# Kernel tuning notes

Measured on AMD Instinct MI355X. Metric: run time of the kernel, lower is better.

The kernel has to match this reference:

```python
import jax, jax.numpy as jnp
import numpy as np

B, S, DIM = 8, 1, 2048
H = 16
QLR, KVLR = 1536, 512
DN, DR, DV = 128, 64, 128      # qk_nope, qk_rope, v head dims
START = 8191                    # start_pos; end_pos = START + S = 8192
EPS = 1e-6
SCALE = (DN + DR) ** -0.5


def _rms(x, w):
    # F.rms_norm: x / sqrt(mean(x^2)+eps) * w
    return x * w * jax.lax.rsqrt(jnp.mean(jnp.square(x), axis=-1, keepdims=True) + EPS)


def _rope(x, cos, sin):
    # x: [..., r]; consecutive pairs (x0,x1) treated as complex, multiplied by cos+i*sin
    xr, xi = x[..., 0::2], x[..., 1::2]
    out_r = xr * cos - xi * sin
    out_i = xr * sin + xi * cos
    return jnp.stack([out_r, out_i], axis=-1).reshape(x.shape)


def setup_inputs() -> dict:
    key = jax.random.key(0)
    ks = jax.random.split(key, 12)
    # rotary tables for the single decode position
    inv_freq = 1.0 / (10000.0 ** (np.arange(0, DR, 2, dtype=np.float32) / DR))  # [DR/2]
    pos = np.arange(START, START + S, dtype=np.float32)[:, None]                # [S,1]
    ang = pos * inv_freq[None, :]                                               # [S, DR/2]
    return {
        "x": jax.random.normal(ks[0], (B, S, DIM), jnp.float32),
        "start_pos": START,
        "freqs_cos": jnp.asarray(np.cos(ang)),
        "freqs_sin": jnp.asarray(np.sin(ang)),
        "kv_cache_prefix": jax.random.normal(ks[1], (B, START, KVLR), jnp.float32),
        "pe_cache_prefix": jax.random.normal(ks[2], (B, START, DR), jnp.float32),
        "wq_a_w": jax.random.normal(ks[3], (QLR, DIM), jnp.float32) * 0.02,
        "wq_a_b": jnp.zeros((QLR,), jnp.float32),
        "q_norm_w": jnp.ones((QLR,), jnp.float32),
        "wq_b_w": jax.random.normal(ks[4], (H * (DN + DR), QLR), jnp.float32) * 0.02,
        "wq_b_b": jnp.zeros((H * (DN + DR),), jnp.float32),
        "wkv_a_w": jax.random.normal(ks[5], (KVLR + DR, DIM), jnp.float32) * 0.02,
        "wkv_a_b": jnp.zeros((KVLR + DR,), jnp.float32),
        "kv_norm_w": jnp.ones((KVLR,), jnp.float32),
        "wkv_b_w": jax.random.normal(ks[6], (H * (DN + DV), KVLR), jnp.float32) * 0.02,
        "wo_w": jax.random.normal(ks[7], (DIM, H * DV), jnp.float32) * 0.02,
        "wo_b": jnp.zeros((DIM,), jnp.float32),
    }


def reference(x, start_pos, freqs_cos, freqs_sin, kv_cache_prefix, pe_cache_prefix,
              wq_a_w, wq_a_b, q_norm_w, wq_b_w, wq_b_b,
              wkv_a_w, wkv_a_b, kv_norm_w, wkv_b_w, wo_w, wo_b):
    b, s, _ = x.shape
    # low-rank query projection
    q = _rms(x @ wq_a_w.T + wq_a_b, q_norm_w) @ wq_b_w.T + wq_b_b
    q = q.reshape(b, s, H, DN + DR)
    q_nope, q_pe = q[..., :DN], q[..., DN:]
    cos = freqs_cos[None, :, None, :]  # [1,s,1,DR/2]
    sin = freqs_sin[None, :, None, :]
    q_pe = _rope(q_pe, cos, sin)
    # compressed KV + rope key branch
    kvpe = x @ wkv_a_w.T + wkv_a_b               # [b,s,KVLR+DR]
    kv, k_pe = kvpe[..., :KVLR], kvpe[..., KVLR:]
    k_pe = _rope(k_pe[:, :, None, :], cos, sin)[:, :, 0, :]
    # weight absorption: project q_nope into latent space through wkv_b's K-part
    wkv_b = wkv_b_w.reshape(H, DN + DV, KVLR)
    q_abs = jnp.einsum('bshd,hdc->bshc', q_nope, wkv_b[:, :DN])
    # append current step to caches
    kv_cache = jnp.concatenate([kv_cache_prefix, _rms(kv, kv_norm_w)], axis=1)  # [b,t,KVLR]
    pe_cache = jnp.concatenate([pe_cache_prefix, k_pe], axis=1)                 # [b,t,DR]
    # attention in latent space (seqlen=1 decode -> no causal mask needed)
    scores = (jnp.einsum('bshc,btc->bsht', q_abs, kv_cache)
              + jnp.einsum('bshr,btr->bsht', q_pe, pe_cache)) * SCALE
    attn = jax.nn.softmax(scores.astype(jnp.float32), axis=-1).astype(x.dtype)
    out = jnp.einsum('bsht,btc->bshc', attn, kv_cache)
    out = jnp.einsum('bshc,hdc->bshd', out, wkv_b[:, DN:])  # V-part of wkv_b
    return out.reshape(b, s, H * DV) @ wo_w.T + wo_b
```

## Files before the change

### kernel.cpp

```cpp
#include <hip/hip_runtime.h>
#include <math.h>

namespace {
constexpr int B_   = 8;
constexpr int DIM_ = 2048;
constexpr int H_   = 16;
constexpr int QLR_ = 1536;
constexpr int KVLR_= 512;
constexpr int DN_  = 128;
constexpr int DR_  = 64;
constexpr int DV_  = 128;
constexpr int TPRE_= 8191;
constexpr int CE_  = 576;
constexpr int NCH_ = 32;
constexpr int CT_  = 256;
constexpr int TS_  = 32;
constexpr int PSTR_= 20;
constexpr float EPS_ = 1e-6f;
constexpr float SCALE_ = 0.07216878364870322f;

constexpr size_t WS_QLAT  = 0;
constexpr size_t WS_KVPE  = WS_QLAT  + (size_t)B_*QLR_;
constexpr size_t WS_KVNEW = WS_KVPE  + (size_t)B_*CE_;
constexpr size_t WS_PENEW = WS_KVNEW + (size_t)B_*KVLR_;
constexpr size_t WS_QRS   = WS_PENEW + (size_t)B_*DR_;
constexpr size_t WS_QNOPE = WS_QRS   + (size_t)B_;
constexpr size_t WS_QT    = WS_QNOPE + (size_t)B_*H_*DN_;
constexpr size_t WS_MLOC  = WS_QT    + (size_t)B_*CE_*H_;
constexpr size_t WS_LLOC  = WS_MLOC  + (size_t)B_*H_*NCH_;
constexpr size_t WS_OUT2  = WS_LLOC  + (size_t)B_*H_*NCH_;
constexpr size_t WS_OPART = WS_OUT2  + (size_t)B_*DIM_;
}

__device__ __forceinline__ void gload16(const float* src, float* ldsDst) {
  __builtin_amdgcn_global_load_lds((const __attribute__((address_space(1))) void*)src,
                                   (__attribute__((address_space(3))) void*)ldsDst,
                                   16, 0, 0);
}

__device__ __forceinline__ float rsum16(float v) {
  int x = __float_as_int(v);
  v += __int_as_float(__builtin_amdgcn_update_dpp(0, x, 0xB1, 0xF, 0xF, true));
  x = __float_as_int(v);
  v += __int_as_float(__builtin_amdgcn_update_dpp(0, x, 0x4E, 0xF, 0xF, true));
  x = __float_as_int(v);
  v += __int_as_float(__builtin_amdgcn_update_dpp(0, x, 0x141, 0xF, 0xF, true));
  x = __float_as_int(v);
  v += __int_as_float(__builtin_amdgcn_update_dpp(0, x, 0x140, 0xF, 0xF, true));
  return v;
}

__global__ __launch_bounds__(256) void mla_k1(const float* __restrict__ x,
                                              const float* __restrict__ wqa,
                                              const float* __restrict__ bqa,
                                              const float* __restrict__ wkva,
                                              const float* __restrict__ bkva,
                                              float* __restrict__ ws) {
  const int w = threadIdx.x >> 6, l = threadIdx.x & 63;
  const int r = blockIdx.x * 4 + w;
  const float* W; const float* bias; float* out; int rr; int ostride;
  if (r < QLR_) { W = wqa;  bias = bqa;  out = ws + WS_QLAT; rr = r;        ostride = QLR_; }
  else          { W = wkva; bias = bkva; out = ws + WS_KVPE; rr = r - QLR_; ostride = CE_;  }
  const float4* wp = (const float4*)(W + (size_t)rr * DIM_);
  const float4* x4 = (const float4*)x;
  float4 wv[8];
#pragma unroll
  for (int j = 0; j < 8; ++j) wv[j] = wp[l + 64 * j];
  float acc[B_];
#pragma unroll
  for (int b = 0; b < B_; ++b) acc[b] = 0.f;
#pragma unroll
  for (int b = 0; b < B_; ++b) {
#pragma unroll
    for (int j = 0; j < 8; ++j) {
      const float4 xv = x4[b * (DIM_ / 4) + l + 64 * j];
      acc[b] = fmaf(wv[j].x, xv.x, fmaf(wv[j].y, xv.y, fmaf(wv[j].z, xv.z, fmaf(wv[j].w, xv.w, acc[b]))));
    }
  }
#pragma unroll
  for (int b = 0; b < B_; ++b)
#pragma unroll
    for (int s = 32; s; s >>= 1) acc[b] += __shfl_xor(acc[b], s);
  if (l == 0) {
    const float b0 = bias[rr];
#pragma unroll
    for (int b = 0; b < B_; ++b) out[b * ostride + rr] = acc[b] + b0;
  }
}

__global__ __launch_bounds__(256) void mla_k2(const float* __restrict__ kvnw,
                                              const float* __restrict__ fcos,
                                              const float* __restrict__ fsin,
                                              float* __restrict__ ws) {
  const int tid = threadIdx.x;
  const int b = tid >> 5, i = tid & 31;
  const float* kvpe = ws + WS_KVPE + b * CE_;
  float ss = 0.f;
#pragma unroll
  for (int j = 0; j < KVLR_ / 32; ++j) { const float v = kvpe[i + 32 * j]; ss = fmaf(v, v, ss); }
#pragma unroll
  for (int s = 16; s; s >>= 1) ss += __shfl_xor(ss, s, 32);
  const float scale = 1.0f / sqrtf(ss / (float)KVLR_ + EPS_);
  float* kvn = ws + WS_KVNEW + b * KVLR_;
#pragma unroll
  for (int j = 0; j < KVLR_ / 32; ++j) {
    const int c = i + 32 * j;
    kvn[c] = kvpe[c] * kvnw[c] * scale;
  }
  {
    const float xr = kvpe[KVLR_ + 2 * i], xi = kvpe[KVLR_ + 2 * i + 1];
    const float c = fcos[i], s = fsin[i];
    float* pen = ws + WS_PENEW + b * DR_;
    pen[2 * i]     = xr * c - xi * s;
    pen[2 * i + 1] = xr * s + xi * c;
  }
  {
    const float* p = ws + WS_QLAT + b * QLR_;
    float sq = 0.f;
#pragma unroll
    for (int j = 0; j < QLR_ / 32; ++j) { const float v = p[i + 32 * j]; sq = fmaf(v, v, sq); }
#pragma unroll
    for (int s = 16; s; s >>= 1) sq += __shfl_xor(sq, s, 32);
    if (i == 0) ws[WS_QRS + b] = 1.0f / sqrtf(sq / (float)QLR_ + EPS_);
  }
}

__global__ __launch_bounds__(256) void mla_k3(const float* __restrict__ qnw,
                                              const float* __restrict__ wqb,
                                              const float* __restrict__ bqb,
                                              const float* __restrict__ fcos,
                                              const float* __restrict__ fsin,
                                              float* __restrict__ ws) {
  const int w = threadIdx.x >> 6, l = threadIdx.x & 63;
  const int r0 = blockIdx.x * 8 + w * 2;
  const float4* w0p = (const float4*)(wqb + (size_t)r0 * QLR_);
  const float4* w1p = (const float4*)(wqb + (size_t)(r0 + 1) * QLR_);
  const float4* g4  = (const float4*)qnw;
  const float4* x4  = (const float4*)(ws + WS_QLAT);
  float4 wg0[6], wg1[6];
#pragma unroll
  for (int j = 0; j < 6; ++j) {
    const int c4 = l + 64 * j;
    const float4 a = w0p[c4], bb = w1p[c4], g = g4[c4];
    wg0[j].x = a.x * g.x; wg0[j].y = a.y * g.y; wg0[j].z = a.z * g.z; wg0[j].w = a.w * g.w;
    wg1[j].x = bb.x * g.x; wg1[j].y = bb.y * g.y; wg1[j].z = bb.z * g.z; wg1[j].w = bb.w * g.w;
  }
  float acc0[B_], acc1[B_];
#pragma unroll
  for (int b = 0; b < B_; ++b) { acc0[b] = 0.f; acc1[b] = 0.f; }
#pragma unroll
  for (int b = 0; b < B_; ++b) {
#pragma unroll
    for (int j = 0; j < 6; ++j) {
      const float4 xv = x4[b * (QLR_ / 4) + l + 64 * j];
      acc0[b] = fmaf(wg0[j].x, xv.x, fmaf(wg0[j].y, xv.y, fmaf(wg0[j].z, xv.z, fmaf(wg0[j].w, xv.w, acc0[b]))));
      acc1[b] = fmaf(wg1[j].x, xv.x, fmaf(wg1[j].y, xv.y, fmaf(wg1[j].z, xv.z, fmaf(wg1[j].w, xv.w, acc1[b]))));
    }
  }
#pragma unroll
  for (int b = 0; b < B_; ++b)
#pragma unroll
    for (int s = 32; s; s >>= 1) {
      acc0[b] += __shfl_xor(acc0[b], s);
      acc1[b] += __shfl_xor(acc1[b], s);
    }
  if (l == 0) {
    const int h = r0 / (DN_ + DR_);
    const int j0 = r0 - h * (DN_ + DR_);
    const float b0 = bqb[r0], b1 = bqb[r0 + 1];
    if (j0 < DN_) {
      float* qn = ws + WS_QNOPE;
#pragma unroll
      for (int b = 0; b < B_; ++b) {
        const float sb = ws[WS_QRS + b];
        qn[(b * H_ + h) * DN_ + j0]     = acc0[b] * sb + b0;
        qn[(b * H_ + h) * DN_ + j0 + 1] = acc1[b] * sb + b1;
      }
    } else {
      const int i = (j0 - DN_) >> 1;
      const float c = fcos[i], s = fsin[i];
      float* qTT = ws + WS_QT;
#pragma unroll
      for (int b = 0; b < B_; ++b) {
        const float sb = ws[WS_QRS + b];
        const float xr = acc0[b] * sb + b0, xi = acc1[b] * sb + b1;
        qTT[((size_t)(b * H_ + h)) * CE_ + KVLR_ + 2 * i]     = xr * c - xi * s;
        qTT[((size_t)(b * H_ + h)) * CE_ + KVLR_ + 2 * i + 1] = xr * s + xi * c;
      }
    }
  }
}

__global__ __launch_bounds__(256) void mla_k4(const float* __restrict__ wkvb,
                                              float* __restrict__ ws) {
  __shared__ float red[7 * 32 * B_];
  const int h = blockIdx.y;
  const int strip = blockIdx.x;
  const int tid = threadIdx.x;
  const int c = tid & 31, dg = tid >> 5;
  const int cg = strip * 32 + c;
  const float* qn = ws + WS_QNOPE;
  float acc[B_];
#pragma unroll
  for (int b = 0; b < B_; ++b) acc[b] = 0.f;
  const float* wp = wkvb + (size_t)h * 256 * KVLR_ + cg;
#pragma unroll
  for (int dd = 0; dd < 16; ++dd) {
    const int d = dg * 16 + dd;
    const float wv = wp[(size_t)d * KVLR_];
#pragma unroll
    for (int b = 0; b < B_; ++b) acc[b] = fmaf(qn[(b * H_ + h) * DN_ + d], wv, acc[b]);
  }
  if (dg > 0) {
#pragma unroll
    for (int b = 0; b < B_; ++b) red[(((dg - 1) * 32) + c) * B_ + b] = acc[b];
  }
  __syncthreads();
  if (dg == 0) {
    float* qTT = ws + WS_QT;
#pragma unroll
    for (int b = 0; b < B_; ++b) {
      float v = acc[b];
#pragma unroll
      for (int g = 0; g < 7; ++g) v += red[(g * 32 + c) * B_ + b];
      qTT[((size_t)(b * H_ + h)) * CE_ + cg] = v;
    }
  }
}

__global__ __launch_bounds__(512) void mla_k5(const float* __restrict__ kvpre,
                                              const float* __restrict__ pepre,
                                              float* __restrict__ ws) {
  __shared__ float kv_lds[2][TS_ * CE_];
  __shared__ float p_lds[TS_ * PSTR_];
  __shared__ float m_st[H_], l_st[H_], f_st[H_];

  const int b = blockIdx.y, chunk = blockIdx.x;
  const int t0 = chunk * CT_;
  const int tid = threadIdx.x;
  const int w = tid >> 6, l = tid & 63;
  const int cs = l & 15;
  const int hl = l >> 4;
  const int tg = w >> 1;
  const int hg = (w & 1) * 4 + hl;
  const int c4p = tid >> 2, h4p = tid & 3;

  const float* kvnew = ws + WS_KVNEW + b * KVLR_;
  const float* penew = ws + WS_PENEW + b * DR_;

  auto stageKV = [&](float* buf, int s) {
    const int ts0 = t0 + s * TS_;
#pragma unroll
    for (int k = 0; k < 9; ++k) {
      const int i = w + 8 * k;
      const int f = i * 64 + l;
      const int tl = f / 144;
      const int c4 = f - tl * 144;
      const int tgl = ts0 + tl;
      const float* src;
      if (tgl < TPRE_) {
        src = (c4 < 128) ? (kvpre + ((size_t)b * TPRE_ + tgl) * KVLR_ + 4 * c4)
                         : (pepre + ((size_t)b * TPRE_ + tgl) * DR_ + 4 * (c4 - 128));
      } else {
        src = (c4 < 128) ? (kvnew + 4 * c4) : (penew + 4 * (c4 - 128));
      }
      gload16(src, buf + (size_t)i * 64 * 4);
    }
  };

  stageKV(kv_lds[0], 0);

  float4 q0v[9], q1v[9];
  {
    const float* qb0 = ws + WS_QT + ((size_t)(b * H_) + 2 * hg) * CE_ + cs * 36;
    const float* qb1 = qb0 + CE_;
#pragma unroll
    for (int j = 0; j < 9; ++j) {
      q0v[j] = *(const float4*)(qb0 + 4 * j);
      q1v[j] = *(const float4*)(qb1 + 4 * j);
    }
  }
  if (tid < H_) { m_st[tid] = -3.4e38f; l_st[tid] = 0.f; }

  float o[4][4];
#pragma unroll
  for (int cc = 0; cc < 4; ++cc)
#pragma unroll
    for (int hh = 0; hh < 4; ++hh) o[cc][hh] = 0.f;

  for (int s = 0; s < CT_ / TS_; ++s) {
    __syncthreads();
    if (s + 1 < CT_ / TS_) stageKV(kv_lds[(s + 1) & 1], s + 1);
    const float* bufc = kv_lds[s & 1];

    {
      const float* kb = bufc + (tg * 8) * CE_ + cs * 36;
#pragma unroll
      for (int tt = 0; tt < 8; ++tt) {
        const float* kr = kb + tt * CE_;
        float a0 = 0.f, a1 = 0.f;
#pragma unroll
        for (int j = 0; j < 9; ++j) {
          const float4 k = *(const float4*)(kr + 4 * j);
          const float4 qa = q0v[j], qc = q1v[j];
          a0 = fmaf(k.x, qa.x, fmaf(k.y, qa.y, fmaf(k.z, qa.z, fmaf(k.w, qa.w, a0))));
          a1 = fmaf(k.x, qc.x, fmaf(k.y, qc.y, fmaf(k.z, qc.z, fmaf(k.w, qc.w, a1))));
        }
        a0 = rsum16(a0);
        a1 = rsum16(a1);
        if (cs == 0) {
          float2 v; v.x = a0 * SCALE_; v.y = a1 * SCALE_;
          *(float2*)(p_lds + (tg * 8 + tt) * PSTR_ + 2 * hg) = v;
        }
      }
    }
    __syncthreads();

    {
      const int h2 = tid >> 5, tl2 = tid & 31;
      const float sv = p_lds[tl2 * PSTR_ + h2];
      float msub = sv;
#pragma unroll
      for (int d = 16; d; d >>= 1) msub = fmaxf(msub, __shfl_xor(msub, d, 32));
      const float mold = m_st[h2];
      const float mnew = fmaxf(mold, msub);
      const float e = __expf(sv - mnew);
      float lsum = e;
#pragma unroll
      for (int d = 16; d; d >>= 1) lsum += __shfl_xor(lsum, d, 32);
      p_lds[tl2 * PSTR_ + h2] = e;
      if (tl2 == 0) {
        const float fac = __expf(mold - mnew);
        f_st[h2] = fac;
        l_st[h2] = l_st[h2] * fac + lsum;
        m_st[h2] = mnew;
      }
    }
    __syncthreads();

    {
      const float4 fv = *(const float4*)(f_st + 4 * h4p);
#pragma unroll
      for (int cc = 0; cc < 4; ++cc) {
        o[cc][0] *= fv.x; o[cc][1] *= fv.y; o[cc][2] *= fv.z; o[cc][3] *= fv.w;
      }
#pragma unroll 8
      for (int t = 0; t < TS_; ++t) {
        const float4 kq = *(const float4*)(bufc + t * CE_ + 4 * c4p);
        const float4 pq = *(const float4*)(p_lds + t * PSTR_ + 4 * h4p);
        o[0][0] = fmaf(pq.x, kq.x, o[0][0]); o[0][1] = fmaf(pq.y, kq.x, o[0][1]);
        o[0][2] = fmaf(pq.z, kq.x, o[0][2]); o[0][3] = fmaf(pq.w, kq.x, o[0][3]);
        o[1][0] = fmaf(pq.x, kq.y, o[1][0]); o[1][1] = fmaf(pq.y, kq.y, o[1][1]);
        o[1][2] = fmaf(pq.z, kq.y, o[1][2]); o[1][3] = fmaf(pq.w, kq.y, o[1][3]);
        o[2][0] = fmaf(pq.x, kq.z, o[2][0]); o[2][1] = fmaf(pq.y, kq.z, o[2][1]);
        o[2][2] = fmaf(pq.z, kq.z, o[2][2]); o[2][3] = fmaf(pq.w, kq.z, o[2][3]);
        o[3][0] = fmaf(pq.x, kq.w, o[3][0]); o[3][1] = fmaf(pq.y, kq.w, o[3][1]);
        o[3][2] = fmaf(pq.z, kq.w, o[3][2]); o[3][3] = fmaf(pq.w, kq.w, o[3][3]);
      }
    }
  }

  {
    float* Op = ws + WS_OPART;
#pragma unroll
    for (int hh = 0; hh < 4; ++hh) {
      const int h = 4 * h4p + hh;
      float4 v;
      v.x = o[0][hh]; v.y = o[1][hh]; v.z = o[2][hh]; v.w = o[3][hh];
      *(float4*)(Op + ((size_t)(b * H_ + h) * NCH_ + chunk) * KVLR_ + 4 * c4p) = v;
    }
    if (tid < H_) {
      ws[WS_MLOC + (b * H_ + tid) * NCH_ + chunk] = m_st[tid];
      ws[WS_LLOC + (b * H_ + tid) * NCH_ + chunk] = l_st[tid];
    }
  }
}

__global__ __launch_bounds__(256) void mla_k6(const float* __restrict__ wkvb,
                                              float* __restrict__ ws) {
  const int h = blockIdx.x, b = blockIdx.y;
  __shared__ float wgt[NCH_];
  __shared__ float ao[KVLR_];
  __shared__ float Linv;
  const int tid = threadIdx.x;
  if (tid < NCH_) {
    const float m = ws[WS_MLOC + (b * H_ + h) * NCH_ + tid];
    float M = m;
#pragma unroll
    for (int s = 16; s; s >>= 1) M = fmaxf(M, __shfl_xor(M, s, 32));
    const float wv = __expf(m - M);
    wgt[tid] = wv;
    float lv = ws[WS_LLOC + (b * H_ + h) * NCH_ + tid] * wv;
#pragma unroll
    for (int s = 16; s; s >>= 1) lv += __shfl_xor(lv, s, 32);
    if (tid == 0) Linv = 1.0f / lv;
  }
  __syncthreads();
  const float* Ob = ws + WS_OPART + (size_t)(b * H_ + h) * NCH_ * KVLR_;
  float s0 = 0.f, s1 = 0.f;
#pragma unroll 4
  for (int i = 0; i < NCH_; ++i) {
    const float wv = wgt[i];
    s0 = fmaf(wv, Ob[(size_t)i * KVLR_ + tid], s0);
    s1 = fmaf(wv, Ob[(size_t)i * KVLR_ + tid + 256], s1);
  }
  const float li = Linv;
  ao[tid] = s0 * li;
  ao[tid + 256] = s1 * li;
  __syncthreads();
  const int v = tid >> 1, half = tid & 1;
  const float* w2 = wkvb + ((size_t)h * 256 + DN_ + v) * KVLR_ + half * 256;
  const float* a = ao + half * 256;
  float s = 0.f;
#pragma unroll
  for (int c = 0; c < 256; c += 4) {
    const float4 wv = *(const float4*)(w2 + c);
    s = fmaf(wv.x, a[c], s);
    s = fmaf(wv.y, a[c + 1], s);
    s = fmaf(wv.z, a[c + 2], s);
    s = fmaf(wv.w, a[c + 3], s);
  }
  s += __shfl_xor(s, 1);
  if (half == 0) ws[WS_OUT2 + b * DIM_ + h * DV_ + v] = s;
}

__global__ __launch_bounds__(256) void mla_k7(const float* __restrict__ wo,
                                              const float* __restrict__ wob,
                                              const float* __restrict__ ws,
                                              float* __restrict__ out) {
  const int w = threadIdx.x >> 6, l = threadIdx.x & 63;
  const int r = blockIdx.x * 4 + w;
  const float4* wp = (const float4*)(wo + (size_t)r * DIM_);
  const float4* x4 = (const float4*)(ws + WS_OUT2);
  float4 wv[8];
#pragma unroll
  for (int j = 0; j < 8; ++j) wv[j] = wp[l + 64 * j];
  float acc[B_];
#pragma unroll
  for (int b = 0; b < B_; ++b) acc[b] = 0.f;
#pragma unroll
  for (int b = 0; b < B_; ++b) {
#pragma unroll
    for (int j = 0; j < 8; ++j) {
      const float4 xv = x4[b * (DIM_ / 4) + l + 64 * j];
      acc[b] = fmaf(wv[j].x, xv.x, fmaf(wv[j].y, xv.y, fmaf(wv[j].z, xv.z, fmaf(wv[j].w, xv.w, acc[b]))));
    }
  }
#pragma unroll
  for (int b = 0; b < B_; ++b)
#pragma unroll
    for (int s = 32; s; s >>= 1) acc[b] += __shfl_xor(acc[b], s);
  if (l == 0) {
    const float b0 = wob[r];
#pragma unroll
    for (int b = 0; b < B_; ++b) out[b * DIM_ + r] = acc[b] + b0;
  }
}

extern "C" void kernel_launch(void* const* d_in, const int* in_sizes, int n_in,
                              void* d_out, int out_size, void* d_ws, size_t ws_size,
                              hipStream_t stream) {
  (void)in_sizes; (void)n_in; (void)out_size; (void)ws_size;
  const float* x     = (const float*)d_in[0];
  const float* fcos  = (const float*)d_in[2];
  const float* fsin  = (const float*)d_in[3];
  const float* kvpre = (const float*)d_in[4];
  const float* pepre = (const float*)d_in[5];
  const float* wqa   = (const float*)d_in[6];
  const float* bqa   = (const float*)d_in[7];
  const float* qnw   = (const float*)d_in[8];
  const float* wqb   = (const float*)d_in[9];
  const float* bqb   = (const float*)d_in[10];
  const float* wkva  = (const float*)d_in[11];
  const float* bkva  = (const float*)d_in[12];
  const float* kvnw  = (const float*)d_in[13];
  const float* wkvb  = (const float*)d_in[14];
  const float* wo    = (const float*)d_in[15];
  const float* wob   = (const float*)d_in[16];
  float* ws  = (float*)d_ws;
  float* out = (float*)d_out;

  mla_k1<<<dim3((QLR_ + CE_) / 4), dim3(256), 0, stream>>>(x, wqa, bqa, wkva, bkva, ws);
  mla_k2<<<dim3(1), dim3(256), 0, stream>>>(kvnw, fcos, fsin, ws);
  mla_k3<<<dim3(H_ * (DN_ + DR_) / 8), dim3(256), 0, stream>>>(qnw, wqb, bqb, fcos, fsin, ws);
  mla_k4<<<dim3(16, H_), dim3(256), 0, stream>>>(wkvb, ws);
  mla_k5<<<dim3(NCH_, B_), dim3(512), 0, stream>>>(kvpre, pepre, ws);
  mla_k6<<<dim3(H_, B_), dim3(256), 0, stream>>>(wkvb, ws);
  mla_k7<<<dim3(DIM_ / 4), dim3(256), 0, stream>>>(wo, wob, ws, out);
}
```

Before: 348.3 us.

## Fuse all MLA decode stages into one cooperative persistent kernel with grid syncs

Replaces the seven separate kernel launches with a single cooperative kernel of 256 blocks of 512 threads that runs every stage in turn, separated by grid.sync(). The KV-cache stream prefetch is issued at kernel start so it overlaps the first projections. The RMS-norm statistics are computed in a separate phase, and the RoPE for the new key is folded into the first projection. The aim is to remove launch overhead and inter-kernel gaps, at the cost of grid-wide barriers and some phases using only part of the grid.

```diff
diff --git a/kernel.cpp b/kernel.cpp
--- a/kernel.cpp
+++ b/kernel.cpp
@@ -1,5 +1,8 @@
 #include <hip/hip_runtime.h>
+#include <hip/hip_cooperative_groups.h>
 #include <math.h>
+
+namespace cg = cooperative_groups;
 
 namespace {
 constexpr int B_   = 8;
@@ -23,8 +26,8 @@
 constexpr size_t WS_KVPE  = WS_QLAT  + (size_t)B_*QLR_;
 constexpr size_t WS_KVNEW = WS_KVPE  + (size_t)B_*CE_;
 constexpr size_t WS_PENEW = WS_KVNEW + (size_t)B_*KVLR_;
-constexpr size_t WS_QRS   = WS_PENEW + (size_t)B_*DR_;
-constexpr size_t WS_QNOPE = WS_QRS   + (size_t)B_;
+constexpr size_t WS_SSQ   = WS_PENEW + (size_t)B_*DR_;
+constexpr size_t WS_QNOPE = WS_SSQ   + 16;
 constexpr size_t WS_QT    = WS_QNOPE + (size_t)B_*H_*DN_;
 constexpr size_t WS_MLOC  = WS_QT    + (size_t)B_*CE_*H_;
 constexpr size_t WS_LLOC  = WS_MLOC  + (size_t)B_*H_*NCH_;
@@ -50,203 +53,29 @@
   return v;
 }
 
-__global__ __launch_bounds__(256) void mla_k1(const float* __restrict__ x,
-                                              const float* __restrict__ wqa,
-                                              const float* __restrict__ bqa,
-                                              const float* __restrict__ wkva,
-                                              const float* __restrict__ bkva,
-                                              float* __restrict__ ws) {
-  const int w = threadIdx.x >> 6, l = threadIdx.x & 63;
-  const int r = blockIdx.x * 4 + w;
-  const float* W; const float* bias; float* out; int rr; int ostride;
-  if (r < QLR_) { W = wqa;  bias = bqa;  out = ws + WS_QLAT; rr = r;        ostride = QLR_; }
-  else          { W = wkva; bias = bkva; out = ws + WS_KVPE; rr = r - QLR_; ostride = CE_;  }
-  const float4* wp = (const float4*)(W + (size_t)rr * DIM_);
-  const float4* x4 = (const float4*)x;
-  float4 wv[8];
-#pragma unroll
-  for (int j = 0; j < 8; ++j) wv[j] = wp[l + 64 * j];
-  float acc[B_];
-#pragma unroll
-  for (int b = 0; b < B_; ++b) acc[b] = 0.f;
-#pragma unroll
-  for (int b = 0; b < B_; ++b) {
-#pragma unroll
-    for (int j = 0; j < 8; ++j) {
-      const float4 xv = x4[b * (DIM_ / 4) + l + 64 * j];
-      acc[b] = fmaf(wv[j].x, xv.x, fmaf(wv[j].y, xv.y, fmaf(wv[j].z, xv.z, fmaf(wv[j].w, xv.w, acc[b]))));
-    }
-  }
-#pragma unroll
-  for (int b = 0; b < B_; ++b)
-#pragma unroll
-    for (int s = 32; s; s >>= 1) acc[b] += __shfl_xor(acc[b], s);
-  if (l == 0) {
-    const float b0 = bias[rr];
-#pragma unroll
-    for (int b = 0; b < B_; ++b) out[b * ostride + rr] = acc[b] + b0;
-  }
-}
-
-__global__ __launch_bounds__(256) void mla_k2(const float* __restrict__ kvnw,
-                                              const float* __restrict__ fcos,
-                                              const float* __restrict__ fsin,
-                                              float* __restrict__ ws) {
-  const int tid = threadIdx.x;
-  const int b = tid >> 5, i = tid & 31;
-  const float* kvpe = ws + WS_KVPE + b * CE_;
-  float ss = 0.f;
-#pragma unroll
-  for (int j = 0; j < KVLR_ / 32; ++j) { const float v = kvpe[i + 32 * j]; ss = fmaf(v, v, ss); }
-#pragma unroll
-  for (int s = 16; s; s >>= 1) ss += __shfl_xor(ss, s, 32);
-  const float scale = 1.0f / sqrtf(ss / (float)KVLR_ + EPS_);
-  float* kvn = ws + WS_KVNEW + b * KVLR_;
-#pragma unroll
-  for (int j = 0; j < KVLR_ / 32; ++j) {
-    const int c = i + 32 * j;
-    kvn[c] = kvpe[c] * kvnw[c] * scale;
-  }
-  {
-    const float xr = kvpe[KVLR_ + 2 * i], xi = kvpe[KVLR_ + 2 * i + 1];
-    const float c = fcos[i], s = fsin[i];
-    float* pen = ws + WS_PENEW + b * DR_;
-    pen[2 * i]     = xr * c - xi * s;
-    pen[2 * i + 1] = xr * s + xi * c;
-  }
-  {
-    const float* p = ws + WS_QLAT + b * QLR_;
-    float sq = 0.f;
-#pragma unroll
-    for (int j = 0; j < QLR_ / 32; ++j) { const float v = p[i + 32 * j]; sq = fmaf(v, v, sq); }
-#pragma unroll
-    for (int s = 16; s; s >>= 1) sq += __shfl_xor(sq, s, 32);
-    if (i == 0) ws[WS_QRS + b] = 1.0f / sqrtf(sq / (float)QLR_ + EPS_);
-  }
-}
-
-__global__ __launch_bounds__(256) void mla_k3(const float* __restrict__ qnw,
-                                              const float* __restrict__ wqb,
-                                              const float* __restrict__ bqb,
-                                              const float* __restrict__ fcos,
-                                              const float* __restrict__ fsin,
-                                              float* __restrict__ ws) {
-  const int w = threadIdx.x >> 6, l = threadIdx.x & 63;
-  const int r0 = blockIdx.x * 8 + w * 2;
-  const float4* w0p = (const float4*)(wqb + (size_t)r0 * QLR_);
-  const float4* w1p = (const float4*)(wqb + (size_t)(r0 + 1) * QLR_);
-  const float4* g4  = (const float4*)qnw;
-  const float4* x4  = (const float4*)(ws + WS_QLAT);
-  float4 wg0[6], wg1[6];
-#pragma unroll
-  for (int j = 0; j < 6; ++j) {
-    const int c4 = l + 64 * j;
-    const float4 a = w0p[c4], bb = w1p[c4], g = g4[c4];
-    wg0[j].x = a.x * g.x; wg0[j].y = a.y * g.y; wg0[j].z = a.z * g.z; wg0[j].w = a.w * g.w;
-    wg1[j].x = bb.x * g.x; wg1[j].y = bb.y * g.y; wg1[j].z = bb.z * g.z; wg1[j].w = bb.w * g.w;
-  }
-  float acc0[B_], acc1[B_];
-#pragma unroll
-  for (int b = 0; b < B_; ++b) { acc0[b] = 0.f; acc1[b] = 0.f; }
-#pragma unroll
-  for (int b = 0; b < B_; ++b) {
-#pragma unroll
-    for (int j = 0; j < 6; ++j) {
-      const float4 xv = x4[b * (QLR_ / 4) + l + 64 * j];
-      acc0[b] = fmaf(wg0[j].x, xv.x, fmaf(wg0[j].y, xv.y, fmaf(wg0[j].z, xv.z, fmaf(wg0[j].w, xv.w, acc0[b]))));
-      acc1[b] = fmaf(wg1[j].x, xv.x, fmaf(wg1[j].y, xv.y, fmaf(wg1[j].z, xv.z, fmaf(wg1[j].w, xv.w, acc1[b]))));
-    }
-  }
-#pragma unroll
-  for (int b = 0; b < B_; ++b)
-#pragma unroll
-    for (int s = 32; s; s >>= 1) {
-      acc0[b] += __shfl_xor(acc0[b], s);
-      acc1[b] += __shfl_xor(acc1[b], s);
-    }
-  if (l == 0) {
-    const int h = r0 / (DN_ + DR_);
-    const int j0 = r0 - h * (DN_ + DR_);
-    const float b0 = bqb[r0], b1 = bqb[r0 + 1];
-    if (j0 < DN_) {
-      float* qn = ws + WS_QNOPE;
-#pragma unroll
-      for (int b = 0; b < B_; ++b) {
-        const float sb = ws[WS_QRS + b];
-        qn[(b * H_ + h) * DN_ + j0]     = acc0[b] * sb + b0;
-        qn[(b * H_ + h) * DN_ + j0 + 1] = acc1[b] * sb + b1;
-      }
-    } else {
-      const int i = (j0 - DN_) >> 1;
-      const float c = fcos[i], s = fsin[i];
-      float* qTT = ws + WS_QT;
-#pragma unroll
-      for (int b = 0; b < B_; ++b) {
-        const float sb = ws[WS_QRS + b];
-        const float xr = acc0[b] * sb + b0, xi = acc1[b] * sb + b1;
-        qTT[((size_t)(b * H_ + h)) * CE_ + KVLR_ + 2 * i]     = xr * c - xi * s;
-        qTT[((size_t)(b * H_ + h)) * CE_ + KVLR_ + 2 * i + 1] = xr * s + xi * c;
-      }
-    }
-  }
-}
-
-__global__ __launch_bounds__(256) void mla_k4(const float* __restrict__ wkvb,
-                                              float* __restrict__ ws) {
-  __shared__ float red[7 * 32 * B_];
-  const int h = blockIdx.y;
-  const int strip = blockIdx.x;
-  const int tid = threadIdx.x;
-  const int c = tid & 31, dg = tid >> 5;
-  const int cg = strip * 32 + c;
-  const float* qn = ws + WS_QNOPE;
-  float acc[B_];
-#pragma unroll
-  for (int b = 0; b < B_; ++b) acc[b] = 0.f;
-  const float* wp = wkvb + (size_t)h * 256 * KVLR_ + cg;
-#pragma unroll
-  for (int dd = 0; dd < 16; ++dd) {
-    const int d = dg * 16 + dd;
-    const float wv = wp[(size_t)d * KVLR_];
-#pragma unroll
-    for (int b = 0; b < B_; ++b) acc[b] = fmaf(qn[(b * H_ + h) * DN_ + d], wv, acc[b]);
-  }
-  if (dg > 0) {
-#pragma unroll
-    for (int b = 0; b < B_; ++b) red[(((dg - 1) * 32) + c) * B_ + b] = acc[b];
-  }
-  __syncthreads();
-  if (dg == 0) {
-    float* qTT = ws + WS_QT;
-#pragma unroll
-    for (int b = 0; b < B_; ++b) {
-      float v = acc[b];
-#pragma unroll
-      for (int g = 0; g < 7; ++g) v += red[(g * 32 + c) * B_ + b];
-      qTT[((size_t)(b * H_ + h)) * CE_ + cg] = v;
-    }
-  }
-}
-
-__global__ __launch_bounds__(512) void mla_k5(const float* __restrict__ kvpre,
-                                              const float* __restrict__ pepre,
-                                              float* __restrict__ ws) {
+__global__ __launch_bounds__(512) void mla_all(
+    const float* __restrict__ x, const float* __restrict__ fcos, const float* __restrict__ fsin,
+    const float* __restrict__ kvpre, const float* __restrict__ pepre,
+    const float* __restrict__ wqa, const float* __restrict__ bqa,
+    const float* __restrict__ qnw, const float* __restrict__ wqb, const float* __restrict__ bqb,
+    const float* __restrict__ wkva, const float* __restrict__ bkva,
+    const float* __restrict__ kvnw, const float* __restrict__ wkvb,
+    const float* __restrict__ wo, const float* __restrict__ wob,
+    float* __restrict__ ws, float* __restrict__ out) {
   __shared__ float kv_lds[2][TS_ * CE_];
   __shared__ float p_lds[TS_ * PSTR_];
   __shared__ float m_st[H_], l_st[H_], f_st[H_];
-
-  const int b = blockIdx.y, chunk = blockIdx.x;
-  const int t0 = chunk * CT_;
+  float* scratch = kv_lds[1];
+
+  cg::grid_group grid = cg::this_grid();
+  const int bid = blockIdx.x;
   const int tid = threadIdx.x;
   const int w = tid >> 6, l = tid & 63;
-  const int cs = l & 15;
-  const int hl = l >> 4;
-  const int tg = w >> 1;
-  const int hg = (w & 1) * 4 + hl;
-  const int c4p = tid >> 2, h4p = tid & 3;
-
-  const float* kvnew = ws + WS_KVNEW + b * KVLR_;
-  const float* penew = ws + WS_PENEW + b * DR_;
+
+  const int chunk = bid & 31, ab = bid >> 5;
+  const int t0 = chunk * CT_;
+  const float* kvraw = ws + WS_KVPE + ab * CE_;
+  const float* penew = ws + WS_PENEW + ab * DR_;
 
   auto stageKV = [&](float* buf, int s) {
     const int ts0 = t0 + s * TS_;
@@ -259,10 +88,10 @@
       const int tgl = ts0 + tl;
       const float* src;
       if (tgl < TPRE_) {
-        src = (c4 < 128) ? (kvpre + ((size_t)b * TPRE_ + tgl) * KVLR_ + 4 * c4)
-                         : (pepre + ((size_t)b * TPRE_ + tgl) * DR_ + 4 * (c4 - 128));
+        src = (c4 < 128) ? (kvpre + ((size_t)ab * TPRE_ + tgl) * KVLR_ + 4 * c4)
+                         : (pepre + ((size_t)ab * TPRE_ + tgl) * DR_ + 4 * (c4 - 128));
       } else {
-        src = (c4 < 128) ? (kvnew + 4 * c4) : (penew + 4 * (c4 - 128));
+        src = (c4 < 128) ? (kvraw + 4 * c4) : (penew + 4 * (c4 - 128));
       }
       gload16(src, buf + (size_t)i * 64 * 4);
     }
@@ -270,190 +99,395 @@
 
   stageKV(kv_lds[0], 0);
 
-  float4 q0v[9], q1v[9];
   {
-    const float* qb0 = ws + WS_QT + ((size_t)(b * H_) + 2 * hg) * CE_ + cs * 36;
-    const float* qb1 = qb0 + CE_;
-#pragma unroll
-    for (int j = 0; j < 9; ++j) {
-      q0v[j] = *(const float4*)(qb0 + 4 * j);
-      q1v[j] = *(const float4*)(qb1 + 4 * j);
-    }
-  }
-  if (tid < H_) { m_st[tid] = -3.4e38f; l_st[tid] = 0.f; }
-
-  float o[4][4];
-#pragma unroll
-  for (int cc = 0; cc < 4; ++cc)
-#pragma unroll
-    for (int hh = 0; hh < 4; ++hh) o[cc][hh] = 0.f;
-
-  for (int s = 0; s < CT_ / TS_; ++s) {
+    const int wid = bid * 8 + w;
+    {
+      const int r = wid;
+      const bool isq = r < QLR_;
+      const float* W = isq ? wqa : wkva;
+      const float* bias = isq ? bqa : bkva;
+      const int rr = isq ? r : r - QLR_;
+      const float4* wp = (const float4*)(W + (size_t)rr * DIM_);
+      const float4* x4 = (const float4*)x;
+      float4 wv[8];
+#pragma unroll
+      for (int j = 0; j < 8; ++j) wv[j] = wp[l + 64 * j];
+      float acc[B_];
+#pragma unroll
+      for (int b = 0; b < B_; ++b) acc[b] = 0.f;
+#pragma unroll
+      for (int b = 0; b < B_; ++b) {
+#pragma unroll
+        for (int j = 0; j < 8; ++j) {
+          const float4 xv = x4[b * (DIM_ / 4) + l + 64 * j];
+          acc[b] = fmaf(wv[j].x, xv.x, fmaf(wv[j].y, xv.y, fmaf(wv[j].z, xv.z, fmaf(wv[j].w, xv.w, acc[b]))));
+        }
+      }
+#pragma unroll
+      for (int b = 0; b < B_; ++b)
+#pragma unroll
+        for (int s = 32; s; s >>= 1) acc[b] += __shfl_xor(acc[b], s);
+      if (l == 0) {
+        const float b0 = bias[rr];
+        if (isq) {
+#pragma unroll
+          for (int b = 0; b < B_; ++b) ws[WS_QLAT + b * QLR_ + rr] = acc[b] + b0;
+        } else {
+#pragma unroll
+          for (int b = 0; b < B_; ++b) ws[WS_KVPE + b * CE_ + rr] = acc[b] + b0;
+        }
+      }
+    }
+    if (wid < 32) {
+      const int rr0 = KVLR_ + 2 * wid;
+      const float4* w0p = (const float4*)(wkva + (size_t)rr0 * DIM_);
+      const float4* w1p = (const float4*)(wkva + (size_t)(rr0 + 1) * DIM_);
+      const float4* x4 = (const float4*)x;
+      float4 wv0[8], wv1[8];
+#pragma unroll
+      for (int j = 0; j < 8; ++j) { wv0[j] = w0p[l + 64 * j]; wv1[j] = w1p[l + 64 * j]; }
+      float a0[B_], a1[B_];
+#pragma unroll
+      for (int b = 0; b < B_; ++b) { a0[b] = 0.f; a1[b] = 0.f; }
+#pragma unroll
+      for (int b = 0; b < B_; ++b) {
+#pragma unroll
+        for (int j = 0; j < 8; ++j) {
+          const float4 xv = x4[b * (DIM_ / 4) + l + 64 * j];
+          a0[b] = fmaf(wv0[j].x, xv.x, fmaf(wv0[j].y, xv.y, fmaf(wv0[j].z, xv.z, fmaf(wv0[j].w, xv.w, a0[b]))));
+          a1[b] = fmaf(wv1[j].x, xv.x, fmaf(wv1[j].y, xv.y, fmaf(wv1[j].z, xv.z, fmaf(wv1[j].w, xv.w, a1[b]))));
+        }
+      }
+#pragma unroll
+      for (int b = 0; b < B_; ++b)
+#pragma unroll
+        for (int s = 32; s; s >>= 1) { a0[b] += __shfl_xor(a0[b], s); a1[b] += __shfl_xor(a1[b], s); }
+      if (l == 0) {
+        const float b0 = bkva[rr0], b1 = bkva[rr0 + 1];
+        const float c = fcos[wid], s = fsin[wid];
+#pragma unroll
+        for (int b = 0; b < B_; ++b) {
+          const float xr = a0[b] + b0, xi = a1[b] + b1;
+          ws[WS_PENEW + b * DR_ + 2 * wid]     = xr * c - xi * s;
+          ws[WS_PENEW + b * DR_ + 2 * wid + 1] = xr * s + xi * c;
+        }
+      }
+    }
+  }
+  grid.sync();
+
+  if (bid < 16) {
+    const int b2 = bid & 7;
+    float ss = 0.f;
+    if (bid < 8) {
+#pragma unroll
+      for (int k = tid; k < QLR_; k += 512) { const float v = ws[WS_QLAT + b2 * QLR_ + k]; ss = fmaf(v, v, ss); }
+    } else {
+      const float v = ws[WS_KVPE + b2 * CE_ + tid]; ss = v * v;
+    }
+#pragma unroll
+    for (int d = 32; d; d >>= 1) ss += __shfl_xor(ss, d);
+    if (l == 0) scratch[w] = ss;
     __syncthreads();
-    if (s + 1 < CT_ / TS_) stageKV(kv_lds[(s + 1) & 1], s + 1);
-    const float* bufc = kv_lds[s & 1];
-
+    if (tid == 0) {
+      float s = 0.f;
+#pragma unroll
+      for (int g = 0; g < 8; ++g) s += scratch[g];
+      const float n = (bid < 8) ? (float)QLR_ : (float)KVLR_;
+      ws[WS_SSQ + (bid < 8 ? b2 : B_ + b2)] = 1.0f / sqrtf(s / n + EPS_);
+    }
+  }
+  grid.sync();
+
+  {
+    const int wid = bid * 8 + w;
+    if (wid < 1536) {
+      const int r0 = 2 * wid;
+      const float4* w0p = (const float4*)(wqb + (size_t)r0 * QLR_);
+      const float4* w1p = (const float4*)(wqb + (size_t)(r0 + 1) * QLR_);
+      const float4* g4  = (const float4*)qnw;
+      const float4* x4  = (const float4*)(ws + WS_QLAT);
+      float4 wg0[6], wg1[6];
+#pragma unroll
+      for (int j = 0; j < 6; ++j) {
+        const int c4 = l + 64 * j;
+        const float4 a = w0p[c4], bb = w1p[c4], g = g4[c4];
+        wg0[j].x = a.x * g.x; wg0[j].y = a.y * g.y; wg0[j].z = a.z * g.z; wg0[j].w = a.w * g.w;
+        wg1[j].x = bb.x * g.x; wg1[j].y = bb.y * g.y; wg1[j].z = bb.z * g.z; wg1[j].w = bb.w * g.w;
+      }
+      float acc0[B_], acc1[B_];
+#pragma unroll
+      for (int b = 0; b < B_; ++b) { acc0[b] = 0.f; acc1[b] = 0.f; }
+#pragma unroll
+      for (int b = 0; b < B_; ++b) {
+#pragma unroll
+        for (int j = 0; j < 6; ++j) {
+          const float4 xv = x4[b * (QLR_ / 4) + l + 64 * j];
+          acc0[b] = fmaf(wg0[j].x, xv.x, fmaf(wg0[j].y, xv.y, fmaf(wg0[j].z, xv.z, fmaf(wg0[j].w, xv.w, acc0[b]))));
+          acc1[b] = fmaf(wg1[j].x, xv.x, fmaf(wg1[j].y, xv.y, fmaf(wg1[j].z, xv.z, fmaf(wg1[j].w, xv.w, acc1[b]))));
+        }
+      }
+#pragma unroll
+      for (int b = 0; b < B_; ++b)
+#pragma unroll
+        for (int s = 32; s; s >>= 1) { acc0[b] += __shfl_xor(acc0[b], s); acc1[b] += __shfl_xor(acc1[b], s); }
+      if (l == 0) {
+        const int h = r0 / (DN_ + DR_);
+        const int j0 = r0 - h * (DN_ + DR_);
+        const float b0 = bqb[r0], b1 = bqb[r0 + 1];
+        if (j0 < DN_) {
+          float* qn = ws + WS_QNOPE;
+#pragma unroll
+          for (int b = 0; b < B_; ++b) {
+            const float sb = ws[WS_SSQ + b];
+            qn[(b * H_ + h) * DN_ + j0]     = acc0[b] * sb + b0;
+            qn[(b * H_ + h) * DN_ + j0 + 1] = acc1[b] * sb + b1;
+          }
+        } else {
+          const int i = (j0 - DN_) >> 1;
+          const float c = fcos[i], s = fsin[i];
+          float* qTT = ws + WS_QT;
+#pragma unroll
+          for (int b = 0; b < B_; ++b) {
+            const float sb = ws[WS_SSQ + b];
+            const float xr = acc0[b] * sb + b0, xi = acc1[b] * sb + b1;
+            qTT[((size_t)(b * H_ + h)) * CE_ + KVLR_ + 2 * i]     = xr * c - xi * s;
+            qTT[((size_t)(b * H_ + h)) * CE_ + KVLR_ + 2 * i + 1] = xr * s + xi * c;
+          }
+        }
+      }
+    }
+  }
+  grid.sync();
+
+  {
+    const int h = bid >> 4, strip = bid & 15;
+    float* red = scratch;
+    const int c = tid & 31, dg = tid >> 5;
+    const int cg = strip * 32 + c;
+    const float* qn = ws + WS_QNOPE;
+    float acc[B_];
+#pragma unroll
+    for (int b = 0; b < B_; ++b) acc[b] = 0.f;
+    const float* wp = wkvb + (size_t)h * 256 * KVLR_ + cg;
+#pragma unroll
+    for (int dd = 0; dd < 8; ++dd) {
+      const int d = dg * 8 + dd;
+      const float wv = wp[(size_t)d * KVLR_];
+#pragma unroll
+      for (int b = 0; b < B_; ++b) acc[b] = fmaf(qn[(b * H_ + h) * DN_ + d], wv, acc[b]);
+    }
+    if (dg > 0) {
+#pragma unroll
+      for (int b = 0; b < B_; ++b) red[(((dg - 1) * 32) + c) * B_ + b] = acc[b];
+    }
+    __syncthreads();
+    if (dg == 0) {
+      float* qTT = ws + WS_QT;
+#pragma unroll
+      for (int b = 0; b < B_; ++b) {
+        float v = acc[b];
+#pragma unroll
+        for (int g = 0; g < 15; ++g) v += red[(g * 32 + c) * B_ + b];
+        qTT[((size_t)(b * H_ + h)) * CE_ + cg] = v;
+      }
+    }
+  }
+  grid.sync();
+
+  {
+    const int cs = l & 15;
+    const int hl = l >> 4;
+    const int tg5 = w >> 1;
+    const int hg = (w & 1) * 4 + hl;
+    const int c4p = tid >> 2, h4p = tid & 3;
+
+    float4 q0v[9], q1v[9];
     {
-      const float* kb = bufc + (tg * 8) * CE_ + cs * 36;
-#pragma unroll
-      for (int tt = 0; tt < 8; ++tt) {
-        const float* kr = kb + tt * CE_;
-        float a0 = 0.f, a1 = 0.f;
-#pragma unroll
-        for (int j = 0; j < 9; ++j) {
-          const float4 k = *(const float4*)(kr + 4 * j);
-          const float4 qa = q0v[j], qc = q1v[j];
-          a0 = fmaf(k.x, qa.x, fmaf(k.y, qa.y, fmaf(k.z, qa.z, fmaf(k.w, qa.w, a0))));
-          a1 = fmaf(k.x, qc.x, fmaf(k.y, qc.y, fmaf(k.z, qc.z, fmaf(k.w, qc.w, a1))));
-        }
-        a0 = rsum16(a0);
-        a1 = rsum16(a1);
-        if (cs == 0) {
-          float2 v; v.x = a0 * SCALE_; v.y = a1 * SCALE_;
-          *(float2*)(p_lds + (tg * 8 + tt) * PSTR_ + 2 * hg) = v;
-        }
-      }
+      const float* qb0 = ws + WS_QT + ((size_t)(ab * H_) + 2 * hg) * CE_ + cs * 36;
+      const float* qb1 = qb0 + CE_;
+#pragma unroll
+      for (int j = 0; j < 9; ++j) { q0v[j] = *(const float4*)(qb0 + 4 * j); q1v[j] = *(const float4*)(qb1 + 4 * j); }
+    }
+    if (tid < H_) { m_st[tid] = -3.4e38f; l_st[tid] = 0.f; }
+
+    float o[4][4];
+#pragma unroll
+    for (int cc = 0; cc < 4; ++cc)
+#pragma unroll
+      for (int hh = 0; hh < 4; ++hh) o[cc][hh] = 0.f;
+
+    for (int s = 0; s < CT_ / TS_; ++s) {
+      __syncthreads();
+      if (s + 1 < CT_ / TS_) stageKV(kv_lds[(s + 1) & 1], s + 1);
+      float* bufc = kv_lds[s & 1];
+
+      if (chunk == NCH_ - 1 && s == CT_ / TS_ - 1) {
+        const float sck = ws[WS_SSQ + B_ + ab];
+        float* row = bufc + (TS_ - 1) * CE_;
+        row[tid] = row[tid] * kvnw[tid] * sck;
+        __syncthreads();
+      }
+
+      {
+        const float* kb = bufc + (tg5 * 8) * CE_ + cs * 36;
+#pragma unroll
+        for (int tt = 0; tt < 8; ++tt) {
+          const float* kr = kb + tt * CE_;
+          float a0 = 0.f, a1 = 0.f;
+#pragma unroll
+          for (int j = 0; j < 9; ++j) {
+            const float4 k = *(const float4*)(kr + 4 * j);
+            const float4 qa = q0v[j], qc = q1v[j];
+            a0 = fmaf(k.x, qa.x, fmaf(k.y, qa.y, fmaf(k.z, qa.z, fmaf(k.w, qa.w, a0))));
+            a1 = fmaf(k.x, qc.x, fmaf(k.y, qc.y, fmaf(k.z, qc.z, fmaf(k.w, qc.w, a1))));
+          }
+          a0 = rsum16(a0);
+          a1 = rsum16(a1);
+          if (cs == 0) {
+            float2 v; v.x = a0 * SCALE_; v.y = a1 * SCALE_;
+            *(float2*)(p_lds + (tg5 * 8 + tt) * PSTR_ + 2 * hg) = v;
+          }
+        }
+      }
+      __syncthreads();
+
+      {
+        const int h2 = tid >> 5, tl2 = tid & 31;
+        const float sv = p_lds[tl2 * PSTR_ + h2];
+        float msub = sv;
+#pragma unroll
+        for (int d = 16; d; d >>= 1) msub = fmaxf(msub, __shfl_xor(msub, d, 32));
+        const float mold = m_st[h2];
+        const float mnew = fmaxf(mold, msub);
+        const float e = __expf(sv - mnew);
+        float lsum = e;
+#pragma unroll
+        for (int d = 16; d; d >>= 1) lsum += __shfl_xor(lsum, d, 32);
+        p_lds[tl2 * PSTR_ + h2] = e;
+        if (tl2 == 0) {
+          const float fac = __expf(mold - mnew);
+          f_st[h2] = fac;
+          l_st[h2] = l_st[h2] * fac + lsum;
+          m_st[h2] = mnew;
+        }
+      }
+      __syncthreads();
+
+      {
+        const float4 fv = *(const float4*)(f_st + 4 * h4p);
+#pragma unroll
+        for (int cc = 0; cc < 4; ++cc) {
+          o[cc][0] *= fv.x; o[cc][1] *= fv.y; o[cc][2] *= fv.z; o[cc][3] *= fv.w;
+        }
+#pragma unroll 8
+        for (int t = 0; t < TS_; ++t) {
+          const float4 kq = *(const float4*)(bufc + t * CE_ + 4 * c4p);
+          const float4 pq = *(const float4*)(p_lds + t * PSTR_ + 4 * h4p);
+          o[0][0] = fmaf(pq.x, kq.x, o[0][0]); o[0][1] = fmaf(pq.y, kq.x, o[0][1]);
+          o[0][2] = fmaf(pq.z, kq.x, o[0][2]); o[0][3] = fmaf(pq.w, kq.x, o[0][3]);
+          o[1][0] = fmaf(pq.x, kq.y, o[1][0]); o[1][1] = fmaf(pq.y, kq.y, o[1][1]);
+          o[1][2] = fmaf(pq.z, kq.y, o[1][2]); o[1][3] = fmaf(pq.w, kq.y, o[1][3]);
+          o[2][0] = fmaf(pq.x, kq.z, o[2][0]); o[2][1] = fmaf(pq.y, kq.z, o[2][1]);
+          o[2][2] = fmaf(pq.z, kq.z, o[2][2]); o[2][3] = fmaf(pq.w, kq.z, o[2][3]);
+          o[3][0] = fmaf(pq.x, kq.w, o[3][0]); o[3][1] = fmaf(pq.y, kq.w, o[3][1]);
+          o[3][2] = fmaf(pq.z, kq.w, o[3][2]); o[3][3] = fmaf(pq.w, kq.w, o[3][3]);
+        }
+      }
+    }
+
+    {
+      float* Op = ws + WS_OPART;
+#pragma unroll
+      for (int hh = 0; hh < 4; ++hh) {
+        const int h = 4 * h4p + hh;
+        float4 v;
+        v.x = o[0][hh]; v.y = o[1][hh]; v.z = o[2][hh]; v.w = o[3][hh];
+        *(float4*)(Op + ((size_t)(ab * H_ + h) * NCH_ + chunk) * KVLR_ + 4 * c4p) = v;
+      }
+      if (tid < H_) {
+        ws[WS_MLOC + (ab * H_ + tid) * NCH_ + chunk] = m_st[tid];
+        ws[WS_LLOC + (ab * H_ + tid) * NCH_ + chunk] = l_st[tid];
+      }
+    }
+  }
+  grid.sync();
+
+  {
+    const int idx = bid >> 1, half6 = bid & 1;
+    const int h = idx & 15, b6 = idx >> 4;
+    float* ao6 = scratch;
+    float* wgt6 = scratch + KVLR_;
+    float* linvp = scratch + KVLR_ + NCH_;
+    if (tid < NCH_) {
+      const float m = ws[WS_MLOC + (b6 * H_ + h) * NCH_ + tid];
+      float M = m;
+#pragma unroll
+      for (int s = 16; s; s >>= 1) M = fmaxf(M, __shfl_xor(M, s, 32));
+      const float wv = __expf(m - M);
+      wgt6[tid] = wv;
+      float lv = ws[WS_LLOC + (b6 * H_ + h) * NCH_ + tid] * wv;
+#pragma unroll
+      for (int s = 16; s; s >>= 1) lv += __shfl_xor(lv, s, 32);
+      if (tid == 0) linvp[0] = 1.0f / lv;
     }
     __syncthreads();
-
-    {
-      const int h2 = tid >> 5, tl2 = tid & 31;
-      const float sv = p_lds[tl2 * PSTR_ + h2];
-      float msub = sv;
-#pragma unroll
-      for (int d = 16; d; d >>= 1) msub = fmaxf(msub, __shfl_xor(msub, d, 32));
-      const float mold = m_st[h2];
-      const float mnew = fmaxf(mold, msub);
-      const float e = __expf(sv - mnew);
-      float lsum = e;
-#pragma unroll
-      for (int d = 16; d; d >>= 1) lsum += __shfl_xor(lsum, d, 32);
-      p_lds[tl2 * PSTR_ + h2] = e;
-      if (tl2 == 0) {
-        const float fac = __expf(mold - mnew);
-        f_st[h2] = fac;
-        l_st[h2] = l_st[h2] * fac + lsum;
-        m_st[h2] = mnew;
-      }
-    }
+    const float* Ob = ws + WS_OPART + (size_t)(b6 * H_ + h) * NCH_ * KVLR_;
+    float s0 = 0.f;
+#pragma unroll 4
+    for (int i = 0; i < NCH_; ++i) s0 = fmaf(wgt6[i], Ob[(size_t)i * KVLR_ + tid], s0);
+    ao6[tid] = s0 * linvp[0];
     __syncthreads();
 
-    {
-      const float4 fv = *(const float4*)(f_st + 4 * h4p);
-#pragma unroll
-      for (int cc = 0; cc < 4; ++cc) {
-        o[cc][0] *= fv.x; o[cc][1] *= fv.y; o[cc][2] *= fv.z; o[cc][3] *= fv.w;
-      }
-#pragma unroll 8
-      for (int t = 0; t < TS_; ++t) {
-        const float4 kq = *(const float4*)(bufc + t * CE_ + 4 * c4p);
-        const float4 pq = *(const float4*)(p_lds + t * PSTR_ + 4 * h4p);
-        o[0][0] = fmaf(pq.x, kq.x, o[0][0]); o[0][1] = fmaf(pq.y, kq.x, o[0][1]);
-        o[0][2] = fmaf(pq.z, kq.x, o[0][2]); o[0][3] = fmaf(pq.w, kq.x, o[0][3]);
-        o[1][0] = fmaf(pq.x, kq.y, o[1][0]); o[1][1] = fmaf(pq.y, kq.y, o[1][1]);
-        o[1][2] = fmaf(pq.z, kq.y, o[1][2]); o[1][3] = fmaf(pq.w, kq.y, o[1][3]);
-        o[2][0] = fmaf(pq.x, kq.z, o[2][0]); o[2][1] = fmaf(pq.y, kq.z, o[2][1]);
-        o[2][2] = fmaf(pq.z, kq.z, o[2][2]); o[2][3] = fmaf(pq.w, kq.z, o[2][3]);
-        o[3][0] = fmaf(pq.x, kq.w, o[3][0]); o[3][1] = fmaf(pq.y, kq.w, o[3][1]);
-        o[3][2] = fmaf(pq.z, kq.w, o[3][2]); o[3][3] = fmaf(pq.w, kq.w, o[3][3]);
-      }
-    }
-  }
+    const int w6 = tid >> 6, l6 = tid & 63;
+    const float4 axv = *(const float4*)(ao6 + 4 * l6);
+    const float4 bxv = *(const float4*)(ao6 + 256 + 4 * l6);
+    float* out2 = ws + WS_OUT2 + b6 * DIM_ + h * DV_;
+#pragma unroll
+    for (int k = 0; k < 8; k += 2) {
+      const int v0 = half6 * 64 + w6 * 8 + k;
+      const float4* w20 = (const float4*)(wkvb + ((size_t)h * 256 + DN_ + v0) * KVLR_);
+      const float4* w21 = (const float4*)(wkvb + ((size_t)h * 256 + DN_ + v0 + 1) * KVLR_);
+      const float4 a0 = w20[l6], c0 = w20[64 + l6];
+      const float4 a1 = w21[l6], c1 = w21[64 + l6];
+      float t0v = fmaf(a0.x, axv.x, fmaf(a0.y, axv.y, fmaf(a0.z, axv.z, fmaf(a0.w, axv.w,
+                  fmaf(c0.x, bxv.x, fmaf(c0.y, bxv.y, fmaf(c0.z, bxv.z, c0.w * bxv.w)))))));
+      float t1v = fmaf(a1.x, axv.x, fmaf(a1.y, axv.y, fmaf(a1.z, axv.z, fmaf(a1.w, axv.w,
+                  fmaf(c1.x, bxv.x, fmaf(c1.y, bxv.y, fmaf(c1.z, bxv.z, c1.w * bxv.w)))))));
+#pragma unroll
+      for (int d = 32; d; d >>= 1) { t0v += __shfl_xor(t0v, d); t1v += __shfl_xor(t1v, d); }
+      if (l6 == 0) { out2[v0] = t0v; out2[v0 + 1] = t1v; }
+    }
+  }
+  grid.sync();
 
   {
-    float* Op = ws + WS_OPART;
-#pragma unroll
-    for (int hh = 0; hh < 4; ++hh) {
-      const int h = 4 * h4p + hh;
-      float4 v;
-      v.x = o[0][hh]; v.y = o[1][hh]; v.z = o[2][hh]; v.w = o[3][hh];
-      *(float4*)(Op + ((size_t)(b * H_ + h) * NCH_ + chunk) * KVLR_ + 4 * c4p) = v;
-    }
-    if (tid < H_) {
-      ws[WS_MLOC + (b * H_ + tid) * NCH_ + chunk] = m_st[tid];
-      ws[WS_LLOC + (b * H_ + tid) * NCH_ + chunk] = l_st[tid];
-    }
-  }
-}
-
-__global__ __launch_bounds__(256) void mla_k6(const float* __restrict__ wkvb,
-                                              float* __restrict__ ws) {
-  const int h = blockIdx.x, b = blockIdx.y;
-  __shared__ float wgt[NCH_];
-  __shared__ float ao[KVLR_];
-  __shared__ float Linv;
-  const int tid = threadIdx.x;
-  if (tid < NCH_) {
-    const float m = ws[WS_MLOC + (b * H_ + h) * NCH_ + tid];
-    float M = m;
-#pragma unroll
-    for (int s = 16; s; s >>= 1) M = fmaxf(M, __shfl_xor(M, s, 32));
-    const float wv = __expf(m - M);
-    wgt[tid] = wv;
-    float lv = ws[WS_LLOC + (b * H_ + h) * NCH_ + tid] * wv;
-#pragma unroll
-    for (int s = 16; s; s >>= 1) lv += __shfl_xor(lv, s, 32);
-    if (tid == 0) Linv = 1.0f / lv;
-  }
-  __syncthreads();
-  const float* Ob = ws + WS_OPART + (size_t)(b * H_ + h) * NCH_ * KVLR_;
-  float s0 = 0.f, s1 = 0.f;
-#pragma unroll 4
-  for (int i = 0; i < NCH_; ++i) {
-    const float wv = wgt[i];
-    s0 = fmaf(wv, Ob[(size_t)i * KVLR_ + tid], s0);
-    s1 = fmaf(wv, Ob[(size_t)i * KVLR_ + tid + 256], s1);
-  }
-  const float li = Linv;
-  ao[tid] = s0 * li;
-  ao[tid + 256] = s1 * li;
-  __syncthreads();
-  const int v = tid >> 1, half = tid & 1;
-  const float* w2 = wkvb + ((size_t)h * 256 + DN_ + v) * KVLR_ + half * 256;
-  const float* a = ao + half * 256;
-  float s = 0.f;
-#pragma unroll
-  for (int c = 0; c < 256; c += 4) {
-    const float4 wv = *(const float4*)(w2 + c);
-    s = fmaf(wv.x, a[c], s);
-    s = fmaf(wv.y, a[c + 1], s);
-    s = fmaf(wv.z, a[c + 2], s);
-    s = fmaf(wv.w, a[c + 3], s);
-  }
-  s += __shfl_xor(s, 1);
-  if (half == 0) ws[WS_OUT2 + b * DIM_ + h * DV_ + v] = s;
-}
-
-__global__ __launch_bounds__(256) void mla_k7(const float* __restrict__ wo,
-                                              const float* __restrict__ wob,
-                                              const float* __restrict__ ws,
-                                              float* __restrict__ out) {
-  const int w = threadIdx.x >> 6, l = threadIdx.x & 63;
-  const int r = blockIdx.x * 4 + w;
-  const float4* wp = (const float4*)(wo + (size_t)r * DIM_);
-  const float4* x4 = (const float4*)(ws + WS_OUT2);
-  float4 wv[8];
-#pragma unroll
-  for (int j = 0; j < 8; ++j) wv[j] = wp[l + 64 * j];
-  float acc[B_];
-#pragma unroll
-  for (int b = 0; b < B_; ++b) acc[b] = 0.f;
-#pragma unroll
-  for (int b = 0; b < B_; ++b) {
-#pragma unroll
-    for (int j = 0; j < 8; ++j) {
-      const float4 xv = x4[b * (DIM_ / 4) + l + 64 * j];
-      acc[b] = fmaf(wv[j].x, xv.x, fmaf(wv[j].y, xv.y, fmaf(wv[j].z, xv.z, fmaf(wv[j].w, xv.w, acc[b]))));
-    }
-  }
-#pragma unroll
-  for (int b = 0; b < B_; ++b)
-#pragma unroll
-    for (int s = 32; s; s >>= 1) acc[b] += __shfl_xor(acc[b], s);
-  if (l == 0) {
-    const float b0 = wob[r];
-#pragma unroll
-    for (int b = 0; b < B_; ++b) out[b * DIM_ + r] = acc[b] + b0;
+    const int r = bid * 8 + w;
+    const float4* wp = (const float4*)(wo + (size_t)r * DIM_);
+    const float4* x4 = (const float4*)(ws + WS_OUT2);
+    float4 wv[8];
+#pragma unroll
+    for (int j = 0; j < 8; ++j) wv[j] = wp[l + 64 * j];
+    float acc[B_];
+#pragma unroll
+    for (int b = 0; b < B_; ++b) acc[b] = 0.f;
+#pragma unroll
+    for (int b = 0; b < B_; ++b) {
+#pragma unroll
+      for (int j = 0; j < 8; ++j) {
+        const float4 xv = x4[b * (DIM_ / 4) + l + 64 * j];
+        acc[b] = fmaf(wv[j].x, xv.x, fmaf(wv[j].y, xv.y, fmaf(wv[j].z, xv.z, fmaf(wv[j].w, xv.w, acc[b]))));
+      }
+    }
+#pragma unroll
+    for (int b = 0; b < B_; ++b)
+#pragma unroll
+      for (int s = 32; s; s >>= 1) acc[b] += __shfl_xor(acc[b], s);
+    if (l == 0) {
+      const float b0 = wob[r];
+#pragma unroll
+      for (int b = 0; b < B_; ++b) out[b * DIM_ + r] = acc[b] + b0;
+    }
   }
 }
 
@@ -480,11 +514,9 @@
   float* ws  = (float*)d_ws;
   float* out = (float*)d_out;
 
-  mla_k1<<<dim3((QLR_ + CE_) / 4), dim3(256), 0, stream>>>(x, wqa, bqa, wkva, bkva, ws);
-  mla_k2<<<dim3(1), dim3(256), 0, stream>>>(kvnw, fcos, fsin, ws);
-  mla_k3<<<dim3(H_ * (DN_ + DR_) / 8), dim3(256), 0, stream>>>(qnw, wqb, bqb, fcos, fsin, ws);
-  mla_k4<<<dim3(16, H_), dim3(256), 0, stream>>>(wkvb, ws);
-  mla_k5<<<dim3(NCH_, B_), dim3(512), 0, stream>>>(kvpre, pepre, ws);
-  mla_k6<<<dim3(H_, B_), dim3(256), 0, stream>>>(wkvb, ws);
-  mla_k7<<<dim3(DIM_ / 4), dim3(256), 0, stream>>>(wo, wob, ws, out);
+  void* args[] = {(void*)&x, (void*)&fcos, (void*)&fsin, (void*)&kvpre, (void*)&pepre,
+                  (void*)&wqa, (void*)&bqa, (void*)&qnw, (void*)&wqb, (void*)&bqb,
+                  (void*)&wkva, (void*)&bkva, (void*)&kvnw, (void*)&wkvb,
+                  (void*)&wo, (void*)&wob, (void*)&ws, (void*)&out};
+  hipLaunchCooperativeKernel((const void*)mla_all, dim3(256), dim3(512), args, 0, stream);
 }
```

Measured after the change: 589.9 us. 69.4% more time.
